# Kernel optimization log

Hardware: AMD Instinct MI355X
Metric: run time of the kernel (lower is better)

The kernel has to match this reference:

```python
import jax, jax.numpy as jnp
import numpy as np

H, DIN, DQ, DK, DV = 16, 1024, 64, 64, 64
B, S = 2, 2048


def setup_inputs() -> dict:
    key = jax.random.key(0)
    ks = jax.random.split(key, 12)
    s_in = 1.0 / np.sqrt(DIN)
    s_cat = 1.0 / np.sqrt(H * DV)
    return {
        "query": jax.random.normal(ks[0], (B, S, DIN), jnp.float32),
        "key_": jax.random.normal(ks[1], (B, S, DIN), jnp.float32),
        "value": jax.random.normal(ks[2], (B, S, DIN), jnp.float32),
        # per-head projection weights stacked on a leading head axis
        "Wq": jax.random.uniform(ks[3], (H, DIN, DQ), jnp.float32, -s_in, s_in),
        "bq": jax.random.uniform(ks[4], (H, DQ), jnp.float32, -s_in, s_in),
        "Wk": jax.random.uniform(ks[5], (H, DIN, DK), jnp.float32, -s_in, s_in),
        "bk": jax.random.uniform(ks[6], (H, DK), jnp.float32, -s_in, s_in),
        "Wv": jax.random.uniform(ks[7], (H, DIN, DV), jnp.float32, -s_in, s_in),
        "bv": jax.random.uniform(ks[8], (H, DV), jnp.float32, -s_in, s_in),
        "Wo": jax.random.uniform(ks[9], (H * DV, DIN), jnp.float32, -s_cat, s_cat),
        "bo": jax.random.uniform(ks[10], (DIN,), jnp.float32, -s_cat, s_cat),
    }


def reference(query, key_, value, Wq, bq, Wk, bk, Wv, bv, Wo, bo):
    # Per-head linear projections, batched over heads: [H,B,S,dh]
    q = jnp.einsum('bsd,hde->hbse', query, Wq) + bq[:, None, None, :]
    k = jnp.einsum('bsd,hde->hbse', key_, Wk) + bk[:, None, None, :]
    v = jnp.einsum('bsd,hde->hbse', value, Wv) + bv[:, None, None, :]
    scale = jnp.float32(DQ) ** 0.5  # query.size(-1) ** 0.5
    scores = jnp.einsum('hbse,hbte->hbst', q, k) / scale  # [H,B,S,S]
    attn = jax.nn.softmax(scores, axis=-1)
    out = jnp.einsum('hbst,hbte->hbse', attn, v)  # [H,B,S,DV]
    # concat heads on feature dim: [B,S,H*DV]
    cat = jnp.transpose(out, (1, 2, 0, 3)).reshape(out.shape[1], out.shape[2], H * DV)
    return cat @ Wo + bo
```

## Files before the change

kernel.cpp:

```cpp
#include <hip/hip_runtime.h>
#include <hip/hip_bf16.h>
#include <cmath>

typedef __bf16 bf16;
typedef bf16 bf16x4 __attribute__((ext_vector_type(4)));
typedef bf16 bf16x8 __attribute__((ext_vector_type(8)));
typedef float f32x4 __attribute__((ext_vector_type(4)));

constexpr int H = 16, DIN = 1024, D = 64, NB = 2, S = 2048;
constexpr int BS = NB * S;
constexpr float LOG2E = 1.4426950408889634f;

__device__ __forceinline__ float exp2_hw(float x) {
#if __has_builtin(__builtin_amdgcn_exp2f)
    return __builtin_amdgcn_exp2f(x);
#else
    return exp2f(x);
#endif
}

__device__ __forceinline__ void gld16(const bf16* g, bf16* lbase, int lane) {
#if __has_builtin(__builtin_amdgcn_global_load_lds)
    __builtin_amdgcn_global_load_lds((const __attribute__((address_space(1))) unsigned int*)g,
                                     (__attribute__((address_space(3))) unsigned int*)lbase,
                                     16, 0, 0);
#else
    *(float4*)((char*)lbase + lane * 16) = *(const float4*)g;
#endif
}

__global__ __launch_bounds__(256) void cvt3_f32_bf16(const float4* __restrict__ in0,
                                                     const float4* __restrict__ in1,
                                                     const float4* __restrict__ in2,
                                                     bf16x4* __restrict__ out0,
                                                     bf16x4* __restrict__ out1,
                                                     bf16x4* __restrict__ out2, int n4) {
    int i = blockIdx.x * 256 + threadIdx.x;
    if (i >= n4) return;
    const float4* in = blockIdx.y == 0 ? in0 : (blockIdx.y == 1 ? in1 : in2);
    bf16x4* out = blockIdx.y == 0 ? out0 : (blockIdx.y == 1 ? out1 : out2);
    float4 v = in[i];
    bf16x4 o = {(bf16)v.x, (bf16)v.y, (bf16)v.z, (bf16)v.w};
    out[i] = o;
}

__global__ __launch_bounds__(256) void transpose3_cvt(const float* __restrict__ w0,
                                                      const float* __restrict__ w1,
                                                      const float* __restrict__ w2,
                                                      bf16* __restrict__ o0,
                                                      bf16* __restrict__ o1,
                                                      bf16* __restrict__ o2) {
    __shared__ float t[32][33];
    int z = blockIdx.z, which = z / H, h = z % H;
    const float* src = (which == 0 ? w0 : (which == 1 ? w1 : w2)) + (long)h * DIN * D;
    bf16* dst = (which == 0 ? o0 : (which == 1 ? o1 : o2)) + (long)h * D * DIN;
    int c0 = blockIdx.x * 32, r0 = blockIdx.y * 32;
    int lx = threadIdx.x & 31, ly = threadIdx.x >> 5;
#pragma unroll
    for (int i = 0; i < 32; i += 8) t[ly + i][lx] = src[(long)(r0 + ly + i) * D + c0 + lx];
    __syncthreads();
#pragma unroll
    for (int i = 0; i < 32; i += 8) dst[(long)(c0 + ly + i) * DIN + r0 + lx] = (bf16)t[lx][ly + i];
}

__global__ __launch_bounds__(256) void transpose_cvt_sq(const float* __restrict__ in,
                                                        bf16* __restrict__ out, int N) {
    __shared__ float t[32][33];
    int c0 = blockIdx.x * 32, r0 = blockIdx.y * 32;
    int lx = threadIdx.x & 31, ly = threadIdx.x >> 5;
#pragma unroll
    for (int i = 0; i < 32; i += 8) t[ly + i][lx] = in[(long)(r0 + ly + i) * N + c0 + lx];
    __syncthreads();
#pragma unroll
    for (int i = 0; i < 32; i += 8) out[(long)(c0 + ly + i) * N + r0 + lx] = (bf16)t[lx][ly + i];
}

__global__ __launch_bounds__(256) void qkv_gemm(const bf16* __restrict__ Aq, const bf16* __restrict__ Ak,
                                                const bf16* __restrict__ Av,
                                                const bf16* __restrict__ Wq_, const bf16* __restrict__ Wk_,
                                                const bf16* __restrict__ Wv_,
                                                const float* __restrict__ bq_, const float* __restrict__ bk_,
                                                const float* __restrict__ bv_,
                                                bf16* __restrict__ Qp, bf16* __restrict__ Kp,
                                                bf16* __restrict__ Vt) {
    __shared__ bf16 As[128 * 32], Bs[128 * 32];
    int lane = threadIdx.x & 63, wid = threadIdx.x >> 6;
    int li = lane & 15, lg = lane >> 4;
    int bx = blockIdx.x, by = blockIdx.y;
    int which = bx >> 3;
    const bf16* A = which == 0 ? Aq : (which == 1 ? Ak : Av);
    const bf16* W = which == 0 ? Wq_ : (which == 1 ? Wk_ : Wv_);
    const float* bias = which == 0 ? bq_ : (which == 1 ? bk_ : bv_);
    float scale = which == 0 ? 0.125f * LOG2E : 1.0f;

    int am0 = by * 128;
    int bn0 = (bx & 7) * 128;
    int srow = lane >> 2, scol = (lane & 3) * 8;

    f32x4 acc[4][4];
#pragma unroll
    for (int i = 0; i < 4; i++)
#pragma unroll
        for (int j = 0; j < 4; j++) acc[i][j] = (f32x4){0.f, 0.f, 0.f, 0.f};

    for (int k0 = 0; k0 < DIN; k0 += 32) {
#pragma unroll
        for (int t = 0; t < 2; t++) {
            int r = (wid * 2 + t) * 16;
            gld16(A + (long)(am0 + r + srow) * DIN + k0 + scol, &As[r * 32], lane);
            gld16(W + (long)(bn0 + r + srow) * DIN + k0 + scol, &Bs[r * 32], lane);
        }
        __syncthreads();
        bf16x8 af[4], bfr[4];
#pragma unroll
        for (int i = 0; i < 4; i++)
            af[i] = *(const bf16x8*)&As[((wid >> 1) * 64 + i * 16 + li) * 32 + lg * 8];
#pragma unroll
        for (int j = 0; j < 4; j++)
            bfr[j] = *(const bf16x8*)&Bs[((wid & 1) * 64 + j * 16 + li) * 32 + lg * 8];
#pragma unroll
        for (int i = 0; i < 4; i++)
#pragma unroll
            for (int j = 0; j < 4; j++)
                acc[i][j] = __builtin_amdgcn_mfma_f32_16x16x32_bf16(af[i], bfr[j], acc[i][j], 0, 0, 0);
        __syncthreads();
    }

#pragma unroll
    for (int i = 0; i < 4; i++) {
#pragma unroll
        for (int j = 0; j < 4; j++) {
            int n = bn0 + (wid & 1) * 64 + j * 16 + li;
            float bv = bias[n];
            int h = n >> 6, e = n & 63;
#pragma unroll
            for (int r = 0; r < 4; r++) {
                int m = am0 + (wid >> 1) * 64 + i * 16 + lg * 4 + r;
                int bb = m >> 11, s = m & 2047;
                float v = (acc[i][j][r] + bv) * scale;
                if (which == 2)
                    Vt[((h * NB + bb) * D + e) * S + s] = (bf16)v;
                else if (which == 0)
                    Qp[((h * NB + bb) * S + s) * D + e] = (bf16)v;
                else
                    Kp[((h * NB + bb) * S + s) * D + e] = (bf16)v;
            }
        }
    }
}

__global__ __launch_bounds__(256) void attn_kernel(const bf16* __restrict__ Qp,
                                                   const bf16* __restrict__ Kp,
                                                   const bf16* __restrict__ VT,
                                                   bf16* __restrict__ cat) {
    __shared__ __align__(16) bf16 plds[4][32][72];
    int lane = threadIdx.x & 63, wid = threadIdx.x >> 6;
    int li = lane & 15, lg = lane >> 4;
    int bid = blockIdx.x;
    int swz = (bid & 7) * 64 + (bid >> 3);
    int hb = swz >> 4, qb = swz & 15;
    int h = hb >> 1, b = hb & 1;
    int q0 = qb * 128 + wid * 32;

    const bf16* Qb = Qp + (long)hb * S * D;
    const bf16* Kb = Kp + (long)hb * S * D;
    const bf16* Vb = VT + (long)hb * D * S;

    bf16x8 qf[2][2];
#pragma unroll
    for (int rf = 0; rf < 2; rf++)
#pragma unroll
        for (int ke = 0; ke < 2; ke++)
            qf[rf][ke] = *(const bf16x8*)(Qb + (q0 + rf * 16 + li) * D + ke * 32 + lg * 8);

    f32x4 o[2][4];
    float mrow[2][4], lrow[2][4];
#pragma unroll
    for (int rf = 0; rf < 2; rf++) {
#pragma unroll
        for (int ef = 0; ef < 4; ef++) o[rf][ef] = (f32x4){0.f, 0.f, 0.f, 0.f};
#pragma unroll
        for (int r = 0; r < 4; r++) { mrow[rf][r] = -INFINITY; lrow[rf][r] = 0.f; }
    }

    for (int t0 = 0; t0 < S; t0 += 64) {
        f32x4 sf[2][4];
#pragma unroll
        for (int rf = 0; rf < 2; rf++)
#pragma unroll
            for (int tf = 0; tf < 4; tf++) sf[rf][tf] = (f32x4){0.f, 0.f, 0.f, 0.f};
        bf16x8 kf[4][2];
#pragma unroll
        for (int tf = 0; tf < 4; tf++)
#pragma unroll
            for (int ke = 0; ke < 2; ke++)
                kf[tf][ke] = *(const bf16x8*)(Kb + (t0 + tf * 16 + li) * D + ke * 32 + lg * 8);
        __builtin_amdgcn_s_setprio(1);
#pragma unroll
        for (int rf = 0; rf < 2; rf++)
#pragma unroll
            for (int tf = 0; tf < 4; tf++)
#pragma unroll
                for (int ke = 0; ke < 2; ke++)
                    sf[rf][tf] = __builtin_amdgcn_mfma_f32_16x16x32_bf16(qf[rf][ke], kf[tf][ke], sf[rf][tf], 0, 0, 0);
        __builtin_amdgcn_s_setprio(0);

        float pm[2][4];
#pragma unroll
        for (int rf = 0; rf < 2; rf++) {
#pragma unroll
            for (int r = 0; r < 4; r++)
                pm[rf][r] = fmaxf(fmaxf(sf[rf][0][r], sf[rf][1][r]), fmaxf(sf[rf][2][r], sf[rf][3][r]));
#pragma unroll
            for (int mask = 1; mask <= 8; mask <<= 1)
#pragma unroll
                for (int r = 0; r < 4; r++) pm[rf][r] = fmaxf(pm[rf][r], __shfl_xor(pm[rf][r], mask));
        }
        float dm = -INFINITY;
#pragma unroll
        for (int rf = 0; rf < 2; rf++)
#pragma unroll
            for (int r = 0; r < 4; r++) dm = fmaxf(dm, pm[rf][r] - mrow[rf][r]);

        if (__all(dm <= 11.5f)) {
#pragma unroll
            for (int rf = 0; rf < 2; rf++) {
                float rs[4] = {0.f, 0.f, 0.f, 0.f};
#pragma unroll
                for (int tf = 0; tf < 4; tf++)
#pragma unroll
                    for (int r = 0; r < 4; r++) {
                        float p = exp2_hw(sf[rf][tf][r] - mrow[rf][r]);
                        sf[rf][tf][r] = p;
                        rs[r] += p;
                    }
#pragma unroll
                for (int mask = 1; mask <= 8; mask <<= 1)
#pragma unroll
                    for (int r = 0; r < 4; r++) rs[r] += __shfl_xor(rs[r], mask);
#pragma unroll
                for (int r = 0; r < 4; r++) lrow[rf][r] += rs[r];
            }
        } else {
#pragma unroll
            for (int rf = 0; rf < 2; rf++) {
                float cr[4];
#pragma unroll
                for (int r = 0; r < 4; r++) {
                    float mn = fmaxf(mrow[rf][r], pm[rf][r]);
                    cr[r] = exp2_hw(mrow[rf][r] - mn);
                    mrow[rf][r] = mn;
                }
                float rs[4] = {0.f, 0.f, 0.f, 0.f};
#pragma unroll
                for (int tf = 0; tf < 4; tf++)
#pragma unroll
                    for (int r = 0; r < 4; r++) {
                        float p = exp2_hw(sf[rf][tf][r] - mrow[rf][r]);
                        sf[rf][tf][r] = p;
                        rs[r] += p;
                    }
#pragma unroll
                for (int mask = 1; mask <= 8; mask <<= 1)
#pragma unroll
                    for (int r = 0; r < 4; r++) rs[r] += __shfl_xor(rs[r], mask);
#pragma unroll
                for (int r = 0; r < 4; r++) lrow[rf][r] = lrow[rf][r] * cr[r] + rs[r];
#pragma unroll
                for (int ef = 0; ef < 4; ef++)
#pragma unroll
                    for (int r = 0; r < 4; r++) o[rf][ef][r] *= cr[r];
            }
        }

#pragma unroll
        for (int rf = 0; rf < 2; rf++)
#pragma unroll
            for (int tf = 0; tf < 4; tf++)
#pragma unroll
                for (int r = 0; r < 4; r++)
                    plds[wid][rf * 16 + lg * 4 + r][tf * 16 + li] = (bf16)sf[rf][tf][r];
        asm volatile("s_waitcnt lgkmcnt(0)" ::: "memory");

        bf16x8 vf[4][2], pf[2][2];
#pragma unroll
        for (int ef = 0; ef < 4; ef++)
#pragma unroll
            for (int ks = 0; ks < 2; ks++)
                vf[ef][ks] = *(const bf16x8*)(Vb + (ef * 16 + li) * S + t0 + ks * 32 + lg * 8);
#pragma unroll
        for (int rf = 0; rf < 2; rf++)
#pragma unroll
            for (int ks = 0; ks < 2; ks++)
                pf[rf][ks] = *(const bf16x8*)&plds[wid][rf * 16 + li][ks * 32 + lg * 8];
        __builtin_amdgcn_s_setprio(1);
#pragma unroll
        for (int rf = 0; rf < 2; rf++)
#pragma unroll
            for (int ef = 0; ef < 4; ef++)
#pragma unroll
                for (int ks = 0; ks < 2; ks++)
                    o[rf][ef] = __builtin_amdgcn_mfma_f32_16x16x32_bf16(pf[rf][ks], vf[ef][ks], o[rf][ef], 0, 0, 0);
        __builtin_amdgcn_s_setprio(0);
    }

#pragma unroll
    for (int rf = 0; rf < 2; rf++)
#pragma unroll
        for (int r = 0; r < 4; r++) {
            float inv = 1.0f / lrow[rf][r];
            int s = q0 + rf * 16 + lg * 4 + r;
#pragma unroll
            for (int ef = 0; ef < 4; ef++)
                cat[((long)b * S + s) * (H * D) + h * D + ef * 16 + li] = (bf16)(o[rf][ef][r] * inv);
        }
}

__global__ __launch_bounds__(256) void out_gemm(const bf16* __restrict__ A,
                                                const bf16* __restrict__ WoT,
                                                const float* __restrict__ bo,
                                                float* __restrict__ out) {
    __shared__ bf16 As[128 * 32], Bs[64 * 32];
    int lane = threadIdx.x & 63, wid = threadIdx.x >> 6;
    int li = lane & 15, lg = lane >> 4;
    int am0 = blockIdx.y * 128, bn0 = blockIdx.x * 64;
    int srow = lane >> 2, scol = (lane & 3) * 8;

    f32x4 acc[4][2];
#pragma unroll
    for (int i = 0; i < 4; i++)
#pragma unroll
        for (int j = 0; j < 2; j++) acc[i][j] = (f32x4){0.f, 0.f, 0.f, 0.f};

    for (int k0 = 0; k0 < DIN; k0 += 32) {
#pragma unroll
        for (int t = 0; t < 2; t++) {
            int r = (wid * 2 + t) * 16;
            gld16(A + (long)(am0 + r + srow) * DIN + k0 + scol, &As[r * 32], lane);
        }
        gld16(WoT + (long)(bn0 + wid * 16 + srow) * DIN + k0 + scol, &Bs[wid * 16 * 32], lane);
        __syncthreads();
        bf16x8 af[4], bfr[2];
#pragma unroll
        for (int i = 0; i < 4; i++)
            af[i] = *(const bf16x8*)&As[((wid >> 1) * 64 + i * 16 + li) * 32 + lg * 8];
#pragma unroll
        for (int j = 0; j < 2; j++)
            bfr[j] = *(const bf16x8*)&Bs[((wid & 1) * 32 + j * 16 + li) * 32 + lg * 8];
#pragma unroll
        for (int i = 0; i < 4; i++)
#pragma unroll
            for (int j = 0; j < 2; j++)
                acc[i][j] = __builtin_amdgcn_mfma_f32_16x16x32_bf16(af[i], bfr[j], acc[i][j], 0, 0, 0);
        __syncthreads();
    }

#pragma unroll
    for (int i = 0; i < 4; i++) {
#pragma unroll
        for (int j = 0; j < 2; j++) {
            int n = bn0 + (wid & 1) * 32 + j * 16 + li;
            float bv = bo[n];
#pragma unroll
            for (int r = 0; r < 4; r++) {
                int m = am0 + (wid >> 1) * 64 + i * 16 + lg * 4 + r;
                out[(long)m * DIN + n] = acc[i][j][r] + bv;
            }
        }
    }
}

extern "C" void kernel_launch(void* const* d_in, const int* in_sizes, int n_in,
                              void* d_out, int out_size, void* d_ws, size_t ws_size,
                              hipStream_t stream) {
    const float* query = (const float*)d_in[0];
    const float* key_  = (const float*)d_in[1];
    const float* value = (const float*)d_in[2];
    const float* Wq = (const float*)d_in[3];
    const float* bq = (const float*)d_in[4];
    const float* Wk = (const float*)d_in[5];
    const float* bk = (const float*)d_in[6];
    const float* Wv = (const float*)d_in[7];
    const float* bv = (const float*)d_in[8];
    const float* Wo = (const float*)d_in[9];
    const float* bo = (const float*)d_in[10];
    float* out = (float*)d_out;

    char* w = (char*)d_ws;
    size_t off = 0;
    auto take = [&](size_t bytes) -> char* {
        char* p = w + off;
        off += (bytes + 255) & ~(size_t)255;
        return p;
    };
    bf16* Xbq = (bf16*)take((size_t)BS * DIN * 2);
    bf16* Xbk = (bf16*)take((size_t)BS * DIN * 2);
    bf16* Xbv = (bf16*)take((size_t)BS * DIN * 2);
    bf16* WqT = (bf16*)take((size_t)H * D * DIN * 2);
    bf16* WkT = (bf16*)take((size_t)H * D * DIN * 2);
    bf16* WvT = (bf16*)take((size_t)H * D * DIN * 2);
    bf16* WoT = (bf16*)take((size_t)DIN * (H * D) * 2);
    bf16* Qp  = (bf16*)take((size_t)H * NB * S * D * 2);
    bf16* Kp  = (bf16*)take((size_t)H * NB * S * D * 2);
    bf16* VTs = (bf16*)take((size_t)H * NB * D * S * 2);
    bf16* cat = (bf16*)take((size_t)BS * (H * D) * 2);

    int n4 = BS * DIN / 4;
    cvt3_f32_bf16<<<dim3(n4 / 256, 3), 256, 0, stream>>>(
        (const float4*)query, (const float4*)key_, (const float4*)value,
        (bf16x4*)Xbq, (bf16x4*)Xbk, (bf16x4*)Xbv, n4);

    transpose3_cvt<<<dim3(D / 32, DIN / 32, 3 * H), 256, 0, stream>>>(Wq, Wk, Wv, WqT, WkT, WvT);
    transpose_cvt_sq<<<dim3(DIN / 32, DIN / 32), 256, 0, stream>>>(Wo, WoT, DIN);

    qkv_gemm<<<dim3(24, 32), 256, 0, stream>>>(Xbq, Xbk, Xbv, WqT, WkT, WvT, bq, bk, bv, Qp, Kp, VTs);

    attn_kernel<<<dim3(512), 256, 0, stream>>>(Qp, Kp, VTs, cat);

    out_gemm<<<dim3(16, 32), 256, 0, stream>>>(cat, WoT, bo, out);
}
```

Measured before the change: 306.1 us.

## Halve attention rows per wave and stage V-transpose stores through LDS

The attention kernel now gives each wave 16 query rows instead of 32 and doubles the grid to 1024 blocks. This lowers register pressure and raises occupancy, but each K/V fragment is now reused over fewer query rows, so global K/V traffic doubles. The QKV GEMM epilogue for V now writes the transposed tile into LDS and then stores contiguous 16-byte vectors to global memory. This replaces the scattered 2-byte strided writes.

```diff
diff --git a/kernel.cpp b/kernel.cpp
--- a/kernel.cpp
+++ b/kernel.cpp
@@ -83,7 +83,9 @@
                                                 const float* __restrict__ bv_,
                                                 bf16* __restrict__ Qp, bf16* __restrict__ Kp,
                                                 bf16* __restrict__ Vt) {
-    __shared__ bf16 As[128 * 32], Bs[128 * 32];
+    __shared__ __align__(16) bf16 smem[128 * 136];
+    bf16* As = smem;
+    bf16* Bs = smem + 128 * 32;
     int lane = threadIdx.x & 63, wid = threadIdx.x >> 6;
     int li = lane & 15, lg = lane >> 4;
     int bx = blockIdx.x, by = blockIdx.y;
@@ -126,24 +128,45 @@
         __syncthreads();
     }
 
-#pragma unroll
-    for (int i = 0; i < 4; i++) {
-#pragma unroll
-        for (int j = 0; j < 4; j++) {
-            int n = bn0 + (wid & 1) * 64 + j * 16 + li;
-            float bv = bias[n];
-            int h = n >> 6, e = n & 63;
-#pragma unroll
-            for (int r = 0; r < 4; r++) {
-                int m = am0 + (wid >> 1) * 64 + i * 16 + lg * 4 + r;
-                int bb = m >> 11, s = m & 2047;
-                float v = (acc[i][j][r] + bv) * scale;
-                if (which == 2)
-                    Vt[((h * NB + bb) * D + e) * S + s] = (bf16)v;
-                else if (which == 0)
-                    Qp[((h * NB + bb) * S + s) * D + e] = (bf16)v;
-                else
-                    Kp[((h * NB + bb) * S + s) * D + e] = (bf16)v;
+    int bb = am0 >> 11;
+    int s0 = am0 & 2047;
+    if (which == 2) {
+#pragma unroll
+        for (int i = 0; i < 4; i++)
+#pragma unroll
+            for (int j = 0; j < 4; j++) {
+                int nl = (wid & 1) * 64 + j * 16 + li;
+                float bv = bias[bn0 + nl];
+#pragma unroll
+                for (int r = 0; r < 4; r++) {
+                    int ml = (wid >> 1) * 64 + i * 16 + lg * 4 + r;
+                    smem[nl * 136 + ml] = (bf16)(acc[i][j][r] + bv);
+                }
+            }
+        __syncthreads();
+        int t = threadIdx.x, row = t >> 1, half = t & 1;
+        int n = bn0 + row, hh = n >> 6, e = n & 63;
+        bf16* dst = Vt + (((long)hh * NB + bb) * D + e) * S + s0 + half * 64;
+        const bf16* srcp = &smem[row * 136 + half * 64];
+#pragma unroll
+        for (int k2 = 0; k2 < 8; k2++)
+            *(bf16x8*)(dst + k2 * 8) = *(const bf16x8*)(srcp + k2 * 8);
+    } else {
+        bf16* outp = which == 0 ? Qp : Kp;
+#pragma unroll
+        for (int i = 0; i < 4; i++) {
+#pragma unroll
+            for (int j = 0; j < 4; j++) {
+                int n = bn0 + (wid & 1) * 64 + j * 16 + li;
+                float bv = bias[n];
+                int h = n >> 6, e = n & 63;
+#pragma unroll
+                for (int r = 0; r < 4; r++) {
+                    int m = am0 + (wid >> 1) * 64 + i * 16 + lg * 4 + r;
+                    int s = m & 2047;
+                    float v = (acc[i][j][r] + bv) * scale;
+                    outp[(((long)h * NB + bb) * S + s) * D + e] = (bf16)v;
+                }
             }
         }
     }
@@ -153,42 +176,35 @@
                                                    const bf16* __restrict__ Kp,
                                                    const bf16* __restrict__ VT,
                                                    bf16* __restrict__ cat) {
-    __shared__ __align__(16) bf16 plds[4][32][72];
+    __shared__ __align__(16) bf16 plds[4][16][72];
     int lane = threadIdx.x & 63, wid = threadIdx.x >> 6;
     int li = lane & 15, lg = lane >> 4;
     int bid = blockIdx.x;
-    int swz = (bid & 7) * 64 + (bid >> 3);
-    int hb = swz >> 4, qb = swz & 15;
+    int swz = (bid & 7) * 128 + (bid >> 3);
+    int hb = swz >> 5, qb = swz & 31;
     int h = hb >> 1, b = hb & 1;
-    int q0 = qb * 128 + wid * 32;
+    int q0 = qb * 64 + wid * 16;
 
     const bf16* Qb = Qp + (long)hb * S * D;
     const bf16* Kb = Kp + (long)hb * S * D;
     const bf16* Vb = VT + (long)hb * D * S;
 
-    bf16x8 qf[2][2];
-#pragma unroll
-    for (int rf = 0; rf < 2; rf++)
-#pragma unroll
-        for (int ke = 0; ke < 2; ke++)
-            qf[rf][ke] = *(const bf16x8*)(Qb + (q0 + rf * 16 + li) * D + ke * 32 + lg * 8);
-
-    f32x4 o[2][4];
-    float mrow[2][4], lrow[2][4];
-#pragma unroll
-    for (int rf = 0; rf < 2; rf++) {
-#pragma unroll
-        for (int ef = 0; ef < 4; ef++) o[rf][ef] = (f32x4){0.f, 0.f, 0.f, 0.f};
-#pragma unroll
-        for (int r = 0; r < 4; r++) { mrow[rf][r] = -INFINITY; lrow[rf][r] = 0.f; }
-    }
+    bf16x8 qf[2];
+#pragma unroll
+    for (int ke = 0; ke < 2; ke++)
+        qf[ke] = *(const bf16x8*)(Qb + (q0 + li) * D + ke * 32 + lg * 8);
+
+    f32x4 o[4];
+    float mrow[4], lrow[4];
+#pragma unroll
+    for (int ef = 0; ef < 4; ef++) o[ef] = (f32x4){0.f, 0.f, 0.f, 0.f};
+#pragma unroll
+    for (int r = 0; r < 4; r++) { mrow[r] = -INFINITY; lrow[r] = 0.f; }
 
     for (int t0 = 0; t0 < S; t0 += 64) {
-        f32x4 sf[2][4];
-#pragma unroll
-        for (int rf = 0; rf < 2; rf++)
-#pragma unroll
-            for (int tf = 0; tf < 4; tf++) sf[rf][tf] = (f32x4){0.f, 0.f, 0.f, 0.f};
+        f32x4 sf[4];
+#pragma unroll
+        for (int tf = 0; tf < 4; tf++) sf[tf] = (f32x4){0.f, 0.f, 0.f, 0.f};
         bf16x8 kf[4][2];
 #pragma unroll
         for (int tf = 0; tf < 4; tf++)
@@ -197,123 +213,102 @@
                 kf[tf][ke] = *(const bf16x8*)(Kb + (t0 + tf * 16 + li) * D + ke * 32 + lg * 8);
         __builtin_amdgcn_s_setprio(1);
 #pragma unroll
-        for (int rf = 0; rf < 2; rf++)
+        for (int tf = 0; tf < 4; tf++)
+#pragma unroll
+            for (int ke = 0; ke < 2; ke++)
+                sf[tf] = __builtin_amdgcn_mfma_f32_16x16x32_bf16(qf[ke], kf[tf][ke], sf[tf], 0, 0, 0);
+        __builtin_amdgcn_s_setprio(0);
+
+        float pm[4];
+#pragma unroll
+        for (int r = 0; r < 4; r++)
+            pm[r] = fmaxf(fmaxf(sf[0][r], sf[1][r]), fmaxf(sf[2][r], sf[3][r]));
+#pragma unroll
+        for (int mask = 1; mask <= 8; mask <<= 1)
+#pragma unroll
+            for (int r = 0; r < 4; r++) pm[r] = fmaxf(pm[r], __shfl_xor(pm[r], mask));
+        float dm = -INFINITY;
+#pragma unroll
+        for (int r = 0; r < 4; r++) dm = fmaxf(dm, pm[r] - mrow[r]);
+
+        if (__all(dm <= 11.5f)) {
+            float rs[4] = {0.f, 0.f, 0.f, 0.f};
 #pragma unroll
             for (int tf = 0; tf < 4; tf++)
 #pragma unroll
-                for (int ke = 0; ke < 2; ke++)
-                    sf[rf][tf] = __builtin_amdgcn_mfma_f32_16x16x32_bf16(qf[rf][ke], kf[tf][ke], sf[rf][tf], 0, 0, 0);
-        __builtin_amdgcn_s_setprio(0);
-
-        float pm[2][4];
-#pragma unroll
-        for (int rf = 0; rf < 2; rf++) {
+                for (int r = 0; r < 4; r++) {
+                    float p = exp2_hw(sf[tf][r] - mrow[r]);
+                    sf[tf][r] = p;
+                    rs[r] += p;
+                }
+#pragma unroll
+            for (int mask = 1; mask <= 8; mask <<= 1)
+#pragma unroll
+                for (int r = 0; r < 4; r++) rs[r] += __shfl_xor(rs[r], mask);
+#pragma unroll
+            for (int r = 0; r < 4; r++) lrow[r] += rs[r];
+        } else {
+            float cr[4];
+#pragma unroll
+            for (int r = 0; r < 4; r++) {
+                float mn = fmaxf(mrow[r], pm[r]);
+                cr[r] = exp2_hw(mrow[r] - mn);
+                mrow[r] = mn;
+            }
+            float rs[4] = {0.f, 0.f, 0.f, 0.f};
+#pragma unroll
+            for (int tf = 0; tf < 4; tf++)
+#pragma unroll
+                for (int r = 0; r < 4; r++) {
+                    float p = exp2_hw(sf[tf][r] - mrow[r]);
+                    sf[tf][r] = p;
+                    rs[r] += p;
+                }
+#pragma unroll
+            for (int mask = 1; mask <= 8; mask <<= 1)
+#pragma unroll
+                for (int r = 0; r < 4; r++) rs[r] += __shfl_xor(rs[r], mask);
+#pragma unroll
+            for (int r = 0; r < 4; r++) lrow[r] = lrow[r] * cr[r] + rs[r];
+#pragma unroll
+            for (int ef = 0; ef < 4; ef++)
+#pragma unroll
+                for (int r = 0; r < 4; r++) o[ef][r] *= cr[r];
+        }
+
+#pragma unroll
+        for (int tf = 0; tf < 4; tf++)
 #pragma unroll
             for (int r = 0; r < 4; r++)
-                pm[rf][r] = fmaxf(fmaxf(sf[rf][0][r], sf[rf][1][r]), fmaxf(sf[rf][2][r], sf[rf][3][r]));
-#pragma unroll
-            for (int mask = 1; mask <= 8; mask <<= 1)
-#pragma unroll
-                for (int r = 0; r < 4; r++) pm[rf][r] = fmaxf(pm[rf][r], __shfl_xor(pm[rf][r], mask));
-        }
-        float dm = -INFINITY;
-#pragma unroll
-        for (int rf = 0; rf < 2; rf++)
-#pragma unroll
-            for (int r = 0; r < 4; r++) dm = fmaxf(dm, pm[rf][r] - mrow[rf][r]);
-
-        if (__all(dm <= 11.5f)) {
-#pragma unroll
-            for (int rf = 0; rf < 2; rf++) {
-                float rs[4] = {0.f, 0.f, 0.f, 0.f};
-#pragma unroll
-                for (int tf = 0; tf < 4; tf++)
-#pragma unroll
-                    for (int r = 0; r < 4; r++) {
-                        float p = exp2_hw(sf[rf][tf][r] - mrow[rf][r]);
-                        sf[rf][tf][r] = p;
-                        rs[r] += p;
-                    }
-#pragma unroll
-                for (int mask = 1; mask <= 8; mask <<= 1)
-#pragma unroll
-                    for (int r = 0; r < 4; r++) rs[r] += __shfl_xor(rs[r], mask);
-#pragma unroll
-                for (int r = 0; r < 4; r++) lrow[rf][r] += rs[r];
-            }
-        } else {
-#pragma unroll
-            for (int rf = 0; rf < 2; rf++) {
-                float cr[4];
-#pragma unroll
-                for (int r = 0; r < 4; r++) {
-                    float mn = fmaxf(mrow[rf][r], pm[rf][r]);
-                    cr[r] = exp2_hw(mrow[rf][r] - mn);
-                    mrow[rf][r] = mn;
-                }
-                float rs[4] = {0.f, 0.f, 0.f, 0.f};
-#pragma unroll
-                for (int tf = 0; tf < 4; tf++)
-#pragma unroll
-                    for (int r = 0; r < 4; r++) {
-                        float p = exp2_hw(sf[rf][tf][r] - mrow[rf][r]);
-                        sf[rf][tf][r] = p;
-                        rs[r] += p;
-                    }
-#pragma unroll
-                for (int mask = 1; mask <= 8; mask <<= 1)
-#pragma unroll
-                    for (int r = 0; r < 4; r++) rs[r] += __shfl_xor(rs[r], mask);
-#pragma unroll
-                for (int r = 0; r < 4; r++) lrow[rf][r] = lrow[rf][r] * cr[r] + rs[r];
-#pragma unroll
-                for (int ef = 0; ef < 4; ef++)
-#pragma unroll
-                    for (int r = 0; r < 4; r++) o[rf][ef][r] *= cr[r];
-            }
-        }
-
-#pragma unroll
-        for (int rf = 0; rf < 2; rf++)
-#pragma unroll
-            for (int tf = 0; tf < 4; tf++)
-#pragma unroll
-                for (int r = 0; r < 4; r++)
-                    plds[wid][rf * 16 + lg * 4 + r][tf * 16 + li] = (bf16)sf[rf][tf][r];
+                plds[wid][lg * 4 + r][tf * 16 + li] = (bf16)sf[tf][r];
         asm volatile("s_waitcnt lgkmcnt(0)" ::: "memory");
 
-        bf16x8 vf[4][2], pf[2][2];
+        bf16x8 vf[4][2], pf[2];
 #pragma unroll
         for (int ef = 0; ef < 4; ef++)
 #pragma unroll
             for (int ks = 0; ks < 2; ks++)
                 vf[ef][ks] = *(const bf16x8*)(Vb + (ef * 16 + li) * S + t0 + ks * 32 + lg * 8);
 #pragma unroll
-        for (int rf = 0; rf < 2; rf++)
+        for (int ks = 0; ks < 2; ks++)
+            pf[ks] = *(const bf16x8*)&plds[wid][li][ks * 32 + lg * 8];
+        __builtin_amdgcn_s_setprio(1);
+#pragma unroll
+        for (int ef = 0; ef < 4; ef++)
 #pragma unroll
             for (int ks = 0; ks < 2; ks++)
-                pf[rf][ks] = *(const bf16x8*)&plds[wid][rf * 16 + li][ks * 32 + lg * 8];
-        __builtin_amdgcn_s_setprio(1);
-#pragma unroll
-        for (int rf = 0; rf < 2; rf++)
-#pragma unroll
-            for (int ef = 0; ef < 4; ef++)
-#pragma unroll
-                for (int ks = 0; ks < 2; ks++)
-                    o[rf][ef] = __builtin_amdgcn_mfma_f32_16x16x32_bf16(pf[rf][ks], vf[ef][ks], o[rf][ef], 0, 0, 0);
+                o[ef] = __builtin_amdgcn_mfma_f32_16x16x32_bf16(pf[ks], vf[ef][ks], o[ef], 0, 0, 0);
         __builtin_amdgcn_s_setprio(0);
     }
 
 #pragma unroll
-    for (int rf = 0; rf < 2; rf++)
-#pragma unroll
-        for (int r = 0; r < 4; r++) {
-            float inv = 1.0f / lrow[rf][r];
-            int s = q0 + rf * 16 + lg * 4 + r;
-#pragma unroll
-            for (int ef = 0; ef < 4; ef++)
-                cat[((long)b * S + s) * (H * D) + h * D + ef * 16 + li] = (bf16)(o[rf][ef][r] * inv);
-        }
+    for (int r = 0; r < 4; r++) {
+        float inv = 1.0f / lrow[r];
+        int s = q0 + lg * 4 + r;
+#pragma unroll
+        for (int ef = 0; ef < 4; ef++)
+            cat[((long)b * S + s) * (H * D) + h * D + ef * 16 + li] = (bf16)(o[ef][r] * inv);
+    }
 }
 
 __global__ __launch_bounds__(256) void out_gemm(const bf16* __restrict__ A,
@@ -415,7 +410,7 @@
 
     qkv_gemm<<<dim3(24, 32), 256, 0, stream>>>(Xbq, Xbk, Xbv, WqT, WkT, WvT, bq, bk, bv, Qp, Kp, VTs);
 
-    attn_kernel<<<dim3(512), 256, 0, stream>>>(Qp, Kp, VTs, cat);
+    attn_kernel<<<dim3(1024), 256, 0, stream>>>(Qp, Kp, VTs, cat);
 
     out_gemm<<<dim3(16, 32), 256, 0, stream>>>(cat, WoT, bo, out);
 }
```

After: 409.8 us. 33.9% more time.

## Double-buffer K/V tiles in LDS for attention and coalesce V-transpose stores

Applied to the files above, without the earlier changes.

The attention kernel now stages each 64-row K and V^T tile into swizzled, double-buffered LDS with asynchronous global-to-LDS loads. The next tile is prefetched while the current one is used, and all four waves share the loads instead of each wave fetching K/V from global memory on its own. The QKV GEMM epilogue for V writes the tile transposed through LDS, so each thread issues contiguous 16-byte stores instead of scattered 2-byte writes. In exchange it adds a block-wide barrier every iteration and uses more LDS, which may lower occupancy.

```diff
diff --git a/kernel.cpp b/kernel.cpp
--- a/kernel.cpp
+++ b/kernel.cpp
@@ -83,7 +83,9 @@
                                                 const float* __restrict__ bv_,
                                                 bf16* __restrict__ Qp, bf16* __restrict__ Kp,
                                                 bf16* __restrict__ Vt) {
-    __shared__ bf16 As[128 * 32], Bs[128 * 32];
+    __shared__ __align__(16) bf16 smem[128 * 136];
+    bf16* As = smem;
+    bf16* Bs = smem + 128 * 32;
     int lane = threadIdx.x & 63, wid = threadIdx.x >> 6;
     int li = lane & 15, lg = lane >> 4;
     int bx = blockIdx.x, by = blockIdx.y;
@@ -126,24 +128,45 @@
         __syncthreads();
     }
 
-#pragma unroll
-    for (int i = 0; i < 4; i++) {
-#pragma unroll
-        for (int j = 0; j < 4; j++) {
-            int n = bn0 + (wid & 1) * 64 + j * 16 + li;
-            float bv = bias[n];
-            int h = n >> 6, e = n & 63;
-#pragma unroll
-            for (int r = 0; r < 4; r++) {
-                int m = am0 + (wid >> 1) * 64 + i * 16 + lg * 4 + r;
-                int bb = m >> 11, s = m & 2047;
-                float v = (acc[i][j][r] + bv) * scale;
-                if (which == 2)
-                    Vt[((h * NB + bb) * D + e) * S + s] = (bf16)v;
-                else if (which == 0)
-                    Qp[((h * NB + bb) * S + s) * D + e] = (bf16)v;
-                else
-                    Kp[((h * NB + bb) * S + s) * D + e] = (bf16)v;
+    int bb = am0 >> 11;
+    int s0 = am0 & 2047;
+    if (which == 2) {
+#pragma unroll
+        for (int i = 0; i < 4; i++)
+#pragma unroll
+            for (int j = 0; j < 4; j++) {
+                int nl = (wid & 1) * 64 + j * 16 + li;
+                float bv = bias[bn0 + nl];
+#pragma unroll
+                for (int r = 0; r < 4; r++) {
+                    int ml = (wid >> 1) * 64 + i * 16 + lg * 4 + r;
+                    smem[nl * 136 + ml] = (bf16)(acc[i][j][r] + bv);
+                }
+            }
+        __syncthreads();
+        int t = threadIdx.x, row = t >> 1, half = t & 1;
+        int n = bn0 + row, hh = n >> 6, e = n & 63;
+        bf16* dst = Vt + (((long)hh * NB + bb) * D + e) * S + s0 + half * 64;
+        const bf16* srcp = &smem[row * 136 + half * 64];
+#pragma unroll
+        for (int k2 = 0; k2 < 8; k2++)
+            *(bf16x8*)(dst + k2 * 8) = *(const bf16x8*)(srcp + k2 * 8);
+    } else {
+        bf16* outp = which == 0 ? Qp : Kp;
+#pragma unroll
+        for (int i = 0; i < 4; i++) {
+#pragma unroll
+            for (int j = 0; j < 4; j++) {
+                int n = bn0 + (wid & 1) * 64 + j * 16 + li;
+                float bv = bias[n];
+                int h = n >> 6, e = n & 63;
+#pragma unroll
+                for (int r = 0; r < 4; r++) {
+                    int m = am0 + (wid >> 1) * 64 + i * 16 + lg * 4 + r;
+                    int s = m & 2047;
+                    float v = (acc[i][j][r] + bv) * scale;
+                    outp[(((long)h * NB + bb) * S + s) * D + e] = (bf16)v;
+                }
             }
         }
     }
@@ -153,6 +176,8 @@
                                                    const bf16* __restrict__ Kp,
                                                    const bf16* __restrict__ VT,
                                                    bf16* __restrict__ cat) {
+    __shared__ __align__(16) bf16 Ks[2][64 * 64];
+    __shared__ __align__(16) bf16 Vs[2][64 * 64];
     __shared__ __align__(16) bf16 plds[4][32][72];
     int lane = threadIdx.x & 63, wid = threadIdx.x >> 6;
     int li = lane & 15, lg = lane >> 4;
@@ -166,6 +191,8 @@
     const bf16* Kb = Kp + (long)hb * S * D;
     const bf16* Vb = VT + (long)hb * D * S;
 
+    int srow8 = lane >> 3, lc16 = (lane & 7) ^ srow8;
+
     bf16x8 qf[2][2];
 #pragma unroll
     for (int rf = 0; rf < 2; rf++)
@@ -183,18 +210,37 @@
         for (int r = 0; r < 4; r++) { mrow[rf][r] = -INFINITY; lrow[rf][r] = 0.f; }
     }
 
+#pragma unroll
+    for (int w = 0; w < 2; w++) {
+        int rb = wid * 16 + w * 8;
+        gld16(Kb + (long)(rb + srow8) * D + lc16 * 8, &Ks[0][rb * 64], lane);
+        gld16(Vb + (long)(rb + srow8) * S + 0 + lc16 * 8, &Vs[0][rb * 64], lane);
+    }
+    __syncthreads();
+    int buf = 0;
+
     for (int t0 = 0; t0 < S; t0 += 64) {
+        if (t0 + 64 < S) {
+#pragma unroll
+            for (int w = 0; w < 2; w++) {
+                int rb = wid * 16 + w * 8;
+                gld16(Kb + (long)(t0 + 64 + rb + srow8) * D + lc16 * 8, &Ks[buf ^ 1][rb * 64], lane);
+                gld16(Vb + (long)(rb + srow8) * S + t0 + 64 + lc16 * 8, &Vs[buf ^ 1][rb * 64], lane);
+            }
+        }
+
+        bf16x8 kf[4][2];
+#pragma unroll
+        for (int tf = 0; tf < 4; tf++)
+#pragma unroll
+            for (int ke = 0; ke < 2; ke++)
+                kf[tf][ke] = *(const bf16x8*)&Ks[buf][(tf * 16 + li) * 64 + (((ke * 4 + lg) ^ (li & 7)) << 3)];
+
         f32x4 sf[2][4];
 #pragma unroll
         for (int rf = 0; rf < 2; rf++)
 #pragma unroll
             for (int tf = 0; tf < 4; tf++) sf[rf][tf] = (f32x4){0.f, 0.f, 0.f, 0.f};
-        bf16x8 kf[4][2];
-#pragma unroll
-        for (int tf = 0; tf < 4; tf++)
-#pragma unroll
-            for (int ke = 0; ke < 2; ke++)
-                kf[tf][ke] = *(const bf16x8*)(Kb + (t0 + tf * 16 + li) * D + ke * 32 + lg * 8);
         __builtin_amdgcn_s_setprio(1);
 #pragma unroll
         for (int rf = 0; rf < 2; rf++)
@@ -287,7 +333,7 @@
         for (int ef = 0; ef < 4; ef++)
 #pragma unroll
             for (int ks = 0; ks < 2; ks++)
-                vf[ef][ks] = *(const bf16x8*)(Vb + (ef * 16 + li) * S + t0 + ks * 32 + lg * 8);
+                vf[ef][ks] = *(const bf16x8*)&Vs[buf][(ef * 16 + li) * 64 + (((ks * 4 + lg) ^ (li & 7)) << 3)];
 #pragma unroll
         for (int rf = 0; rf < 2; rf++)
 #pragma unroll
@@ -302,6 +348,9 @@
                 for (int ks = 0; ks < 2; ks++)
                     o[rf][ef] = __builtin_amdgcn_mfma_f32_16x16x32_bf16(pf[rf][ks], vf[ef][ks], o[rf][ef], 0, 0, 0);
         __builtin_amdgcn_s_setprio(0);
+
+        __syncthreads();
+        buf ^= 1;
     }
 
 #pragma unroll
```

New measurement: 289.8 us. 1.06x faster.
